# Kernel tuning notes

Hardware: AMD Instinct MI355X
Metric: run time of the kernel (lower is better)

The kernel has to match this reference:

```python
import jax, jax.numpy as jnp
import numpy as np

N = 100000
E = 1600000
FEAT = 128
EMBED = 128
CLASSES = 40


def _sage_conv(x, src, dst, W_l, W_r, b, n_nodes):
    # PyG SAGEConv (mean aggr): out = mean_{j in N(i)} x_j @ W_l + x_i @ W_r + b
    msg = x[src]                                                  # [E, d] gather
    agg = jax.ops.segment_sum(msg, dst, num_segments=n_nodes)     # [N, d]
    cnt = jax.ops.segment_sum(jnp.ones((src.shape[0], 1), x.dtype), dst,
                              num_segments=n_nodes)               # [N, 1]
    agg = agg / jnp.maximum(cnt, 1.0)                             # mean (0 for isolated)
    return agg @ W_l + x @ W_r + b


def setup_inputs() -> dict:
    key = jax.random.key(0)
    ks = jax.random.split(key, 10)
    s = lambda d: 1.0 / np.sqrt(d)
    x = jax.random.normal(ks[0], (N, FEAT), dtype=jnp.float32)
    edge_index = jax.random.randint(ks[1], (2, E), 0, N, dtype=jnp.int64)
    W1_l = jax.random.uniform(ks[2], (FEAT, EMBED), jnp.float32, -s(FEAT), s(FEAT))
    W1_r = jax.random.uniform(ks[3], (FEAT, EMBED), jnp.float32, -s(FEAT), s(FEAT))
    b1 = jnp.zeros((EMBED,), jnp.float32)
    W2_l = jax.random.uniform(ks[4], (EMBED, EMBED), jnp.float32, -s(EMBED), s(EMBED))
    W2_r = jax.random.uniform(ks[5], (EMBED, EMBED), jnp.float32, -s(EMBED), s(EMBED))
    b2 = jnp.zeros((EMBED,), jnp.float32)
    W_out = jax.random.uniform(ks[6], (EMBED, CLASSES), jnp.float32, -s(EMBED), s(EMBED))
    b_out = jax.random.uniform(ks[7], (CLASSES,), jnp.float32, -s(EMBED), s(EMBED))
    return {"x": x, "edge_index": edge_index,
            "W1_l": W1_l, "W1_r": W1_r, "b1": b1,
            "W2_l": W2_l, "W2_r": W2_r, "b2": b2,
            "W_out": W_out, "b_out": b_out}


def reference(x, edge_index, W1_l, W1_r, b1, W2_l, W2_r, b2, W_out, b_out):
    src, dst = edge_index[0], edge_index[1]
    n = x.shape[0]
    h = _sage_conv(x, src, dst, W1_l, W1_r, b1, n)   # [N, EMBED]
    h = _sage_conv(h, src, dst, W2_l, W2_r, b2, n)   # [N, EMBED]
    g = jnp.mean(h, axis=0, keepdims=True)           # global_mean_pool, batch=None -> [1, EMBED]
    return g @ W_out + b_out                          # [1, CLASSES]
```

## Files before the change

### kernel.cpp

```cpp
#include <hip/hip_runtime.h>


#define NN    100000
#define NE    1600000
#define NE4   (NE/4)
#define FEAT  128
#define NCLS  40

#define RSC   25000
#define NRC   4
#define NCC   64
#define PERC  6250

#define RSV   16000
#define NRV   7
#define NCV   32
#define PERV  12500

#define SLICE 200
#define FSG   500
#define P1S   400
#define NV    (3*FEAT + 1)
#define NQ    (P1S / 4)
#define NG    10


__global__ __launch_bounds__(1024) void k_cnt8(const int4* __restrict__ dst4,
                                               unsigned* __restrict__ pc) {
    __shared__ unsigned tab[RSC / 4];
    const int c = blockIdx.x, r = blockIdx.y;
    for (int j = threadIdx.x; j < RSC / 4; j += 1024) tab[j] = 0u;
    __syncthreads();
    const int base = r * RSC;
    const int i0 = c * PERC;
    for (int i = i0 + (int)threadIdx.x; i < i0 + PERC; i += 1024) {
        int4 d = dst4[i];
        unsigned a;
        a = (unsigned)(d.x - base); if (a < RSC) atomicAdd(&tab[a >> 2], 1u << ((a & 3) * 8));
        a = (unsigned)(d.y - base); if (a < RSC) atomicAdd(&tab[a >> 2], 1u << ((a & 3) * 8));
        a = (unsigned)(d.z - base); if (a < RSC) atomicAdd(&tab[a >> 2], 1u << ((a & 3) * 8));
        a = (unsigned)(d.w - base); if (a < RSC) atomicAdd(&tab[a >> 2], 1u << ((a & 3) * 8));
    }
    __syncthreads();
    unsigned* outp = pc + (size_t)(r * NCC + c) * (RSC / 4);
    for (int j = threadIdx.x; j < RSC / 4; j += 1024) outp[j] = tab[j];
}

__global__ __launch_bounds__(256) void k_inv(const unsigned* __restrict__ pc,
                                             float* __restrict__ invc) {
    int i = blockIdx.x * 256 + threadIdx.x;
    if (i >= NN) return;
    int rr = i / RSC, jj = i - rr * RSC;
    const unsigned* p = pc + (size_t)rr * NCC * (RSC / 4) + (jj >> 2);
    const unsigned sh = (unsigned)(jj & 3) * 8u;
    unsigned cn = 0;
    #pragma unroll 16
    for (int c = 0; c < NCC; ++c) cn += (p[(size_t)c * (RSC / 4)] >> sh) & 0xFFu;
    invc[i] = 1.0f / (float)(cn > 0u ? cn : 1u);
}


__global__ __launch_bounds__(1024) void k_scat(const int4* __restrict__ src4,
                                               const int4* __restrict__ dst4,
                                               const float* __restrict__ val,
                                               float* __restrict__ partial) {
    __shared__ float tab[RSV];
    const int c = blockIdx.x, r = blockIdx.y;
    for (int j = threadIdx.x; j < RSV; j += 1024) tab[j] = 0.f;
    __syncthreads();
    const int base = r * RSV;
    const int i0 = c * PERV;
    for (int i = i0 + (int)threadIdx.x; i < i0 + PERV; i += 1024) {
        int4 s = src4[i];
        int4 d = dst4[i];
        unsigned a;
        a = (unsigned)(s.x - base); if (a < RSV) atomicAdd(&tab[a], val[d.x]);
        a = (unsigned)(s.y - base); if (a < RSV) atomicAdd(&tab[a], val[d.y]);
        a = (unsigned)(s.z - base); if (a < RSV) atomicAdd(&tab[a], val[d.z]);
        a = (unsigned)(s.w - base); if (a < RSV) atomicAdd(&tab[a], val[d.w]);
    }
    __syncthreads();
    float* outp = partial + (size_t)(r * NCV + c) * RSV;
    for (int j = threadIdx.x; j < RSV; j += 1024) outp[j] = tab[j];
}

__global__ __launch_bounds__(256) void k_mws(const float* __restrict__ partial,
                                             const float* __restrict__ invc,
                                             float* __restrict__ ws, float* __restrict__ u) {
    int i = blockIdx.x * 256 + threadIdx.x;
    if (i >= NN) return;
    int rr = i / RSV, jj = i - rr * RSV;
    const float* p = partial + (size_t)rr * NCV * RSV + jj;
    float w = 0.f;
    #pragma unroll
    for (int c = 0; c < NCV; ++c) w += p[(size_t)c * RSV];
    ws[i] = w;
    u[i] = w * invc[i];
}


__global__ __launch_bounds__(1024) void k_fsm(const float* __restrict__ x,
                                              const float* __restrict__ ws,
                                              const float* __restrict__ partial,
                                              float* __restrict__ p1) {
    __shared__ float t_sl[SLICE], ws_sl[SLICE];
    __shared__ float shx[32][32][4], shw[32][32][4], sht[32][32][4], wsh[32];
    const int bid = blockIdx.x, tid = threadIdx.x;
    const int i0 = bid * SLICE;
    const int rr = bid / (RSV / SLICE);
    const int jj0 = i0 - rr * RSV;

    if (tid < SLICE) {
        const float* p = partial + (size_t)rr * NCV * RSV + (jj0 + tid);
        float tv = 0.f;
        #pragma unroll
        for (int c = 0; c < NCV; ++c) tv += p[(size_t)c * RSV];
        t_sl[tid] = tv;
        ws_sl[tid] = ws[i0 + tid];
    }
    __syncthreads();

    const int lane = tid & 31;
    const int grp  = tid >> 5;
    float sx0=0,sx1=0,sx2=0,sx3=0;
    float sw0=0,sw1=0,sw2=0,sw3=0;
    float st0=0,st1=0,st2=0,st3=0;
    float wsum = 0.f;
    for (int r = grp; r < SLICE; r += 32) {
        const float4* xr = (const float4*)(x + (size_t)(i0 + r) * FEAT);
        float4 v = xr[lane];
        float wr = ws_sl[r];
        float tr = t_sl[r];
        sx0 += v.x; sx1 += v.y; sx2 += v.z; sx3 += v.w;
        sw0 += wr*v.x; sw1 += wr*v.y; sw2 += wr*v.z; sw3 += wr*v.w;
        st0 += tr*v.x; st1 += tr*v.y; st2 += tr*v.z; st3 += tr*v.w;
        if (lane == 0) wsum += wr;
    }
    shx[grp][lane][0]=sx0; shx[grp][lane][1]=sx1; shx[grp][lane][2]=sx2; shx[grp][lane][3]=sx3;
    shw[grp][lane][0]=sw0; shw[grp][lane][1]=sw1; shw[grp][lane][2]=sw2; shw[grp][lane][3]=sw3;
    sht[grp][lane][0]=st0; sht[grp][lane][1]=st1; sht[grp][lane][2]=st2; sht[grp][lane][3]=st3;
    if (lane == 0) wsh[grp] = wsum;
    __syncthreads();

    if (grp == 0) {
        float ax[4]={0,0,0,0}, aw[4]={0,0,0,0}, at[4]={0,0,0,0};
        for (int g = 0; g < 32; ++g) {
            #pragma unroll
            for (int cc = 0; cc < 4; ++cc) {
                ax[cc] += shx[g][lane][cc];
                aw[cc] += shw[g][lane][cc];
                at[cc] += sht[g][lane][cc];
            }
        }
        float* row = p1 + (size_t)bid * P1S;
        #pragma unroll
        for (int cc = 0; cc < 4; ++cc) {
            row[        4*lane + cc] = ax[cc];
            row[FEAT  + 4*lane + cc] = aw[cc];
            row[2*FEAT+ 4*lane + cc] = at[cc];
        }
        if (lane == 0) {
            float w = 0.f;
            for (int g = 0; g < 32; ++g) w += wsh[g];
            row[3*FEAT] = w;
        }
    }
}


__global__ __launch_bounds__(1024) void k_fin(const float* __restrict__ p1,
                                              const float* __restrict__ W1l, const float* __restrict__ W1r,
                                              const float* __restrict__ b1,
                                              const float* __restrict__ W2l, const float* __restrict__ W2r,
                                              const float* __restrict__ b2,
                                              const float* __restrict__ Wout, const float* __restrict__ bout,
                                              float* __restrict__ out) {
    __shared__ float part[NG][P1S];
    __shared__ float fin[800];
    const int tid = threadIdx.x;

    if (tid < NG * NQ) {
        const int g = tid / NQ;
        const int q = tid - g * NQ;
        const float4* p4 = (const float4*)p1;
        float4 a0 = {0,0,0,0}, a1 = {0,0,0,0};
        const int b0 = g * (FSG / NG);
        #pragma unroll 5
        for (int b = b0; b < b0 + FSG / NG; b += 2) {
            float4 v0 = p4[(size_t)b * NQ + q];
            float4 v1 = p4[(size_t)(b + 1) * NQ + q];
            a0.x += v0.x; a0.y += v0.y; a0.z += v0.z; a0.w += v0.w;
            a1.x += v1.x; a1.y += v1.y; a1.z += v1.z; a1.w += v1.w;
        }
        part[g][4*q    ] = a0.x + a1.x;
        part[g][4*q + 1] = a0.y + a1.y;
        part[g][4*q + 2] = a0.z + a1.z;
        part[g][4*q + 3] = a0.w + a1.w;
    }
    __syncthreads();
    if (tid < NV) {
        float s = 0.f;
        #pragma unroll
        for (int g = 0; g < NG; ++g) s += part[g][tid];
        fin[tid] = s;
    }
    __syncthreads();

    if (tid < FEAT) {
        float m1 = (float)NN * b1[tid];
        float s2 = fin[384] * b1[tid];
        for (int k = 0; k < FEAT; ++k) {
            float wl = W1l[k*FEAT + tid];
            float wr = W1r[k*FEAT + tid];
            m1 += fin[128 + k] * wl + fin[k] * wr;
            s2 += fin[256 + k] * wl + fin[128 + k] * wr;
        }
        fin[400 + tid] = m1;
        fin[528 + tid] = s2;
    }
    __syncthreads();
    if (tid < FEAT) {
        float g = 0.f;
        for (int k = 0; k < FEAT; ++k)
            g += fin[528 + k] * W2l[k*FEAT + tid] + fin[400 + k] * W2r[k*FEAT + tid];
        fin[656 + tid] = g * (1.0f / (float)NN) + b2[tid];
    }
    __syncthreads();
    if (tid < NCLS) {
        float o = bout[tid];
        for (int k = 0; k < FEAT; ++k)
            o += fin[656 + k] * Wout[k*NCLS + tid];
        out[tid] = o;
    }
}


__global__ __launch_bounds__(256) void k_count_dev(const int4* __restrict__ dst4, int* __restrict__ cnt) {
    int i = blockIdx.x * 256 + threadIdx.x;
    if (i >= NE4) return;
    int4 d = dst4[i];
    atomicAdd(&cnt[d.x], 1); atomicAdd(&cnt[d.y], 1);
    atomicAdd(&cnt[d.z], 1); atomicAdd(&cnt[d.w], 1);
}

__global__ __launch_bounds__(256) void k_inv_dev(const int* __restrict__ cnt, float* __restrict__ invc) {
    int i = blockIdx.x * 256 + threadIdx.x;
    if (i >= NN) return;
    int c = cnt[i];
    invc[i] = 1.0f / (float)(c > 0 ? c : 1);
}

__global__ __launch_bounds__(256) void k_ws_dev(const int4* __restrict__ src4, const int4* __restrict__ dst4,
                                                const float* __restrict__ invc, float* __restrict__ ws) {
    int i = blockIdx.x * 256 + threadIdx.x;
    if (i >= NE4) return;
    int4 s = src4[i];
    int4 d = dst4[i];
    atomicAdd(&ws[s.x], invc[d.x]); atomicAdd(&ws[s.y], invc[d.y]);
    atomicAdd(&ws[s.z], invc[d.z]); atomicAdd(&ws[s.w], invc[d.w]);
}

__global__ __launch_bounds__(256) void k_u_dev(const float* __restrict__ ws, const float* __restrict__ invc,
                                               float* __restrict__ u) {
    int i = blockIdx.x * 256 + threadIdx.x;
    if (i >= NN) return;
    u[i] = ws[i] * invc[i];
}

__global__ __launch_bounds__(256) void k_t_dev(const int4* __restrict__ src4, const int4* __restrict__ dst4,
                                               const float* __restrict__ u, float* __restrict__ t) {
    int i = blockIdx.x * 256 + threadIdx.x;
    if (i >= NE4) return;
    int4 s = src4[i];
    int4 d = dst4[i];
    atomicAdd(&t[s.x], u[d.x]); atomicAdd(&t[s.y], u[d.y]);
    atomicAdd(&t[s.z], u[d.z]); atomicAdd(&t[s.w], u[d.w]);
}

__global__ __launch_bounds__(256) void k_fs_atom(const float* __restrict__ x,
                                                 const float* __restrict__ ws,
                                                 const float* __restrict__ t,
                                                 float* __restrict__ sums) {
    int lane = threadIdx.x & 31;
    int grp  = threadIdx.x >> 5;
    int row0 = blockIdx.x * 8 + grp;
    int rstride = gridDim.x * 8;
    float sx0=0,sx1=0,sx2=0,sx3=0, sw0=0,sw1=0,sw2=0,sw3=0, st0=0,st1=0,st2=0,st3=0, wsum=0.f;
    for (int r = row0; r < NN; r += rstride) {
        const float4* xr = (const float4*)(x + (size_t)r * FEAT);
        float4 v = xr[lane];
        float wr = ws[r], tr = t[r];
        sx0+=v.x; sx1+=v.y; sx2+=v.z; sx3+=v.w;
        sw0+=wr*v.x; sw1+=wr*v.y; sw2+=wr*v.z; sw3+=wr*v.w;
        st0+=tr*v.x; st1+=tr*v.y; st2+=tr*v.z; st3+=tr*v.w;
        if (lane==0) wsum += wr;
    }
    __shared__ float shx[8][32][4], shw[8][32][4], sht[8][32][4], shwsum[8];
    shx[grp][lane][0]=sx0; shx[grp][lane][1]=sx1; shx[grp][lane][2]=sx2; shx[grp][lane][3]=sx3;
    shw[grp][lane][0]=sw0; shw[grp][lane][1]=sw1; shw[grp][lane][2]=sw2; shw[grp][lane][3]=sw3;
    sht[grp][lane][0]=st0; sht[grp][lane][1]=st1; sht[grp][lane][2]=st2; sht[grp][lane][3]=st3;
    if (lane==0) shwsum[grp]=wsum;
    __syncthreads();
    if (grp==0) {
        float ax[4], aw[4], at[4];
        #pragma unroll
        for (int c=0;c<4;++c){ax[c]=shx[0][lane][c];aw[c]=shw[0][lane][c];at[c]=sht[0][lane][c];}
        #pragma unroll
        for (int g=1;g<8;++g)
            #pragma unroll
            for (int c=0;c<4;++c){ax[c]+=shx[g][lane][c];aw[c]+=shw[g][lane][c];at[c]+=sht[g][lane][c];}
        #pragma unroll
        for (int c=0;c<4;++c){
            atomicAdd(&sums[        4*lane+c], ax[c]);
            atomicAdd(&sums[FEAT  + 4*lane+c], aw[c]);
            atomicAdd(&sums[2*FEAT+ 4*lane+c], at[c]);
        }
        if (lane==0){
            float w=shwsum[0];
            #pragma unroll
            for (int g=1;g<8;++g) w+=shwsum[g];
            atomicAdd(&sums[3*FEAT], w);
        }
    }
}

__global__ __launch_bounds__(128) void k_final_dev(const float* __restrict__ sums,
                                                   const float* __restrict__ W1l, const float* __restrict__ W1r,
                                                   const float* __restrict__ b1,
                                                   const float* __restrict__ W2l, const float* __restrict__ W2r,
                                                   const float* __restrict__ b2,
                                                   const float* __restrict__ Wout, const float* __restrict__ bout,
                                                   float* __restrict__ out) {
    __shared__ float Sx[FEAT], Sw[FEAT], St[FEAT], M1[FEAT], S2[FEAT], G[FEAT];
    __shared__ float Wsum;
    int f = threadIdx.x;
    Sx[f] = sums[f];
    Sw[f] = sums[FEAT + f];
    St[f] = sums[2*FEAT + f];
    if (f == 0) Wsum = sums[3*FEAT];
    __syncthreads();
    float m1 = (float)NN * b1[f];
    float s2 = Wsum * b1[f];
    for (int k = 0; k < FEAT; ++k) {
        float wl = W1l[k*FEAT + f];
        float wr = W1r[k*FEAT + f];
        m1 += Sw[k]*wl + Sx[k]*wr;
        s2 += St[k]*wl + Sw[k]*wr;
    }
    M1[f] = m1; S2[f] = s2;
    __syncthreads();
    float g = 0.f;
    for (int k = 0; k < FEAT; ++k)
        g += S2[k]*W2l[k*FEAT + f] + M1[k]*W2r[k*FEAT + f];
    g = g * (1.0f/(float)NN) + b2[f];
    G[f] = g;
    __syncthreads();
    if (f < NCLS) {
        float o = bout[f];
        for (int k = 0; k < FEAT; ++k)
            o += G[k]*Wout[k*NCLS + f];
        out[f] = o;
    }
}


extern "C" void kernel_launch(void* const* d_in, const int* in_sizes, int n_in,
                              void* d_out, int out_size, void* d_ws, size_t ws_size,
                              hipStream_t stream) {
    const float* x    = (const float*)d_in[0];
    const int*   ei   = (const int*)d_in[1];
    const float* W1l  = (const float*)d_in[2];
    const float* W1r  = (const float*)d_in[3];
    const float* b1   = (const float*)d_in[4];
    const float* W2l  = (const float*)d_in[5];
    const float* W2r  = (const float*)d_in[6];
    const float* b2   = (const float*)d_in[7];
    const float* Wout = (const float*)d_in[8];
    const float* bout = (const float*)d_in[9];
    float* out = (float*)d_out;

    const int4* src4 = (const int4*)ei;
    const int4* dst4 = (const int4*)(ei + NE);

    const size_t PART = (size_t)NRV * NCV * RSV;
    const size_t P1N  = (size_t)FSG * P1S;
    const size_t need = (PART + (size_t)3*NN + P1N) * 4;

    if (ws_size >= need) {
        float* partial = (float*)d_ws;
        float* invc = partial + PART;
        float* ws   = invc + NN;
        float* u    = ws + NN;
        float* p1   = u + NN;

        const int NB = (NN + 255) / 256;

        k_cnt8<<<dim3(NCC, NRC), 1024, 0, stream>>>(dst4, (unsigned*)partial);
        k_inv<<<NB, 256, 0, stream>>>((const unsigned*)partial, invc);
        k_scat<<<dim3(NCV, NRV), 1024, 0, stream>>>(src4, dst4, invc, partial);
        k_mws<<<NB, 256, 0, stream>>>(partial, invc, ws, u);
        k_scat<<<dim3(NCV, NRV), 1024, 0, stream>>>(src4, dst4, u, partial);
        k_fsm<<<FSG, 1024, 0, stream>>>(x, ws, partial, p1);
        k_fin<<<1, 1024, 0, stream>>>(p1, W1l, W1r, b1, W2l, W2r, b2, Wout, bout, out);
    } else {
        int*   cnt  = (int*)d_ws;
        float* wsv  = (float*)d_ws + NN;
        float* t    = (float*)d_ws + 2*NN;
        float* sums = (float*)d_ws + 3*NN;
        float* invc = (float*)d_ws + 3*NN + 640;
        float* u    = (float*)d_ws + 3*NN + 640 + NN;

        hipMemsetAsync(d_ws, 0, ((size_t)3*NN + 640) * 4, stream);

        const int EB4 = (NE4 + 255) / 256;
        const int NB  = (NN + 255) / 256;
        k_count_dev<<<EB4, 256, 0, stream>>>(dst4, cnt);
        k_inv_dev<<<NB, 256, 0, stream>>>(cnt, invc);
        k_ws_dev<<<EB4, 256, 0, stream>>>(src4, dst4, invc, wsv);
        k_u_dev<<<NB, 256, 0, stream>>>(wsv, invc, u);
        k_t_dev<<<EB4, 256, 0, stream>>>(src4, dst4, u, t);
        k_fs_atom<<<256, 256, 0, stream>>>(x, wsv, t, sums);
        k_final_dev<<<1, 128, 0, stream>>>(sums, W1l, W1r, b1, W2l, W2r, b2, Wout, bout, out);
    }
}
```

Before: 185.7 us.

## Fuse final reduction into k_fsm via last-block pattern and vectorize count/mean kernels

```diff
diff --git a/kernel.cpp b/kernel.cpp
--- a/kernel.cpp
+++ b/kernel.cpp
@@ -26,9 +26,11 @@
 
 
 __global__ __launch_bounds__(1024) void k_cnt8(const int4* __restrict__ dst4,
-                                               unsigned* __restrict__ pc) {
+                                               unsigned* __restrict__ pc,
+                                               unsigned* __restrict__ done) {
     __shared__ unsigned tab[RSC / 4];
     const int c = blockIdx.x, r = blockIdx.y;
+    if (c == 0 && r == 0 && threadIdx.x == 0) *done = 0u;
     for (int j = threadIdx.x; j < RSC / 4; j += 1024) tab[j] = 0u;
     __syncthreads();
     const int base = r * RSC;
@@ -46,17 +48,29 @@
     for (int j = threadIdx.x; j < RSC / 4; j += 1024) outp[j] = tab[j];
 }
 
-__global__ __launch_bounds__(256) void k_inv(const unsigned* __restrict__ pc,
-                                             float* __restrict__ invc) {
-    int i = blockIdx.x * 256 + threadIdx.x;
-    if (i >= NN) return;
-    int rr = i / RSC, jj = i - rr * RSC;
+__global__ __launch_bounds__(256) void k_inv4(const unsigned* __restrict__ pc,
+                                              float* __restrict__ invc) {
+    int i4 = blockIdx.x * 256 + threadIdx.x;
+    if (i4 >= NN / 4) return;
+    const int n0 = i4 * 4;
+    const int rr = n0 / RSC;
+    const int jj = n0 - rr * RSC;
     const unsigned* p = pc + (size_t)rr * NCC * (RSC / 4) + (jj >> 2);
-    const unsigned sh = (unsigned)(jj & 3) * 8u;
-    unsigned cn = 0;
+    unsigned acc02 = 0u, acc13 = 0u;
     #pragma unroll 16
-    for (int c = 0; c < NCC; ++c) cn += (p[(size_t)c * (RSC / 4)] >> sh) & 0xFFu;
-    invc[i] = 1.0f / (float)(cn > 0u ? cn : 1u);
+    for (int c = 0; c < NCC; ++c) {
+        unsigned w = p[(size_t)c * (RSC / 4)];
+        acc02 += w & 0x00FF00FFu;
+        acc13 += (w >> 8) & 0x00FF00FFu;
+    }
+    unsigned c0 = acc02 & 0xFFFFu, c2 = acc02 >> 16;
+    unsigned c1 = acc13 & 0xFFFFu, c3 = acc13 >> 16;
+    float4 v;
+    v.x = 1.0f / (float)(c0 > 0u ? c0 : 1u);
+    v.y = 1.0f / (float)(c1 > 0u ? c1 : 1u);
+    v.z = 1.0f / (float)(c2 > 0u ? c2 : 1u);
+    v.w = 1.0f / (float)(c3 > 0u ? c3 : 1u);
+    ((float4*)invc)[i4] = v;
 }
 
 
@@ -84,40 +98,67 @@
     for (int j = threadIdx.x; j < RSV; j += 1024) outp[j] = tab[j];
 }
 
-__global__ __launch_bounds__(256) void k_mws(const float* __restrict__ partial,
-                                             const float* __restrict__ invc,
-                                             float* __restrict__ ws, float* __restrict__ u) {
-    int i = blockIdx.x * 256 + threadIdx.x;
-    if (i >= NN) return;
-    int rr = i / RSV, jj = i - rr * RSV;
-    const float* p = partial + (size_t)rr * NCV * RSV + jj;
-    float w = 0.f;
-    #pragma unroll
-    for (int c = 0; c < NCV; ++c) w += p[(size_t)c * RSV];
-    ws[i] = w;
-    u[i] = w * invc[i];
+__global__ __launch_bounds__(256) void k_mws4(const float* __restrict__ partial,
+                                              const float* __restrict__ invc,
+                                              float* __restrict__ ws, float* __restrict__ u) {
+    int i4 = blockIdx.x * 256 + threadIdx.x;
+    if (i4 >= NN / 4) return;
+    const int n0 = i4 * 4;
+    const int rr = n0 / RSV;
+    const int jj = n0 - rr * RSV;
+    const float4* p = (const float4*)(partial + (size_t)rr * NCV * RSV + jj);
+    float4 w = {0.f, 0.f, 0.f, 0.f};
+    #pragma unroll 8
+    for (int c = 0; c < NCV; ++c) {
+        float4 v = p[(size_t)c * (RSV / 4)];
+        w.x += v.x; w.y += v.y; w.z += v.z; w.w += v.w;
+    }
+    ((float4*)ws)[i4] = w;
+    float4 ic = ((const float4*)invc)[i4];
+    float4 uu = {w.x * ic.x, w.y * ic.y, w.z * ic.z, w.w * ic.w};
+    ((float4*)u)[i4] = uu;
 }
 
 
 __global__ __launch_bounds__(1024) void k_fsm(const float* __restrict__ x,
                                               const float* __restrict__ ws,
                                               const float* __restrict__ partial,
-                                              float* __restrict__ p1) {
-    __shared__ float t_sl[SLICE], ws_sl[SLICE];
-    __shared__ float shx[32][32][4], shw[32][32][4], sht[32][32][4], wsh[32];
+                                              float* __restrict__ p1,
+                                              unsigned* __restrict__ done,
+                                              const float* __restrict__ W1l, const float* __restrict__ W1r,
+                                              const float* __restrict__ b1,
+                                              const float* __restrict__ W2l, const float* __restrict__ W2r,
+                                              const float* __restrict__ b2,
+                                              const float* __restrict__ Wout, const float* __restrict__ bout,
+                                              float* __restrict__ out) {
+    __shared__ float smem[13520];
+    __shared__ unsigned s_last;
+    float* t_sl  = smem;
+    float* ws_sl = smem + 200;
+    float* wsh   = smem + 400;
+    float* tpart = smem + 432;
+    float* shx   = smem + 1232;
+    float* shw   = smem + 5328;
+    float* sht   = smem + 9424;
+
     const int bid = blockIdx.x, tid = threadIdx.x;
     const int i0 = bid * SLICE;
     const int rr = bid / (RSV / SLICE);
     const int jj0 = i0 - rr * RSV;
 
-    if (tid < SLICE) {
-        const float* p = partial + (size_t)rr * NCV * RSV + (jj0 + tid);
+    if (tid < 4 * SLICE) {
+        const int g = tid / SLICE;
+        const int n = tid - g * SLICE;
+        const float* p = partial + (size_t)rr * NCV * RSV + (size_t)(g * 8) * RSV + (jj0 + n);
         float tv = 0.f;
         #pragma unroll
-        for (int c = 0; c < NCV; ++c) tv += p[(size_t)c * RSV];
-        t_sl[tid] = tv;
-        ws_sl[tid] = ws[i0 + tid];
-    }
+        for (int c = 0; c < 8; ++c) tv += p[(size_t)c * RSV];
+        tpart[g * SLICE + n] = tv;
+    }
+    if (tid < SLICE) ws_sl[tid] = ws[i0 + tid];
+    __syncthreads();
+    if (tid < SLICE)
+        t_sl[tid] = tpart[tid] + tpart[SLICE + tid] + tpart[2 * SLICE + tid] + tpart[3 * SLICE + tid];
     __syncthreads();
 
     const int lane = tid & 31;
@@ -136,9 +177,12 @@
         st0 += tr*v.x; st1 += tr*v.y; st2 += tr*v.z; st3 += tr*v.w;
         if (lane == 0) wsum += wr;
     }
-    shx[grp][lane][0]=sx0; shx[grp][lane][1]=sx1; shx[grp][lane][2]=sx2; shx[grp][lane][3]=sx3;
-    shw[grp][lane][0]=sw0; shw[grp][lane][1]=sw1; shw[grp][lane][2]=sw2; shw[grp][lane][3]=sw3;
-    sht[grp][lane][0]=st0; sht[grp][lane][1]=st1; sht[grp][lane][2]=st2; sht[grp][lane][3]=st3;
+    float* px = shx + grp * 128 + lane * 4;
+    float* pw = shw + grp * 128 + lane * 4;
+    float* pt = sht + grp * 128 + lane * 4;
+    px[0]=sx0; px[1]=sx1; px[2]=sx2; px[3]=sx3;
+    pw[0]=sw0; pw[1]=sw1; pw[2]=sw2; pw[3]=sw3;
+    pt[0]=st0; pt[1]=st1; pt[2]=st2; pt[3]=st3;
     if (lane == 0) wsh[grp] = wsum;
     __syncthreads();
 
@@ -147,9 +191,9 @@
         for (int g = 0; g < 32; ++g) {
             #pragma unroll
             for (int cc = 0; cc < 4; ++cc) {
-                ax[cc] += shx[g][lane][cc];
-                aw[cc] += shw[g][lane][cc];
-                at[cc] += sht[g][lane][cc];
+                ax[cc] += shx[g*128 + lane*4 + cc];
+                aw[cc] += shw[g*128 + lane*4 + cc];
+                at[cc] += sht[g*128 + lane*4 + cc];
             }
         }
         float* row = p1 + (size_t)bid * P1S;
@@ -165,19 +209,22 @@
             row[3*FEAT] = w;
         }
     }
-}
-
-
-__global__ __launch_bounds__(1024) void k_fin(const float* __restrict__ p1,
-                                              const float* __restrict__ W1l, const float* __restrict__ W1r,
-                                              const float* __restrict__ b1,
-                                              const float* __restrict__ W2l, const float* __restrict__ W2r,
-                                              const float* __restrict__ b2,
-                                              const float* __restrict__ Wout, const float* __restrict__ bout,
-                                              float* __restrict__ out) {
-    __shared__ float part[NG][P1S];
-    __shared__ float fin[800];
-    const int tid = threadIdx.x;
+    __syncthreads();
+
+    if (tid == 0) {
+        __threadfence();
+        unsigned old = atomicAdd(done, 1u);
+        s_last = (old == (unsigned)(FSG - 1)) ? 1u : 0u;
+    }
+    __syncthreads();
+    if (!s_last) return;
+    __threadfence();
+
+    float* part = smem;
+    float* fin  = smem + 4000;
+    float* pm   = smem + 4800;
+    float* ps   = smem + 5824;
+    float* po   = smem + 6848;
 
     if (tid < NG * NQ) {
         const int g = tid / NQ;
@@ -192,44 +239,73 @@
             a0.x += v0.x; a0.y += v0.y; a0.z += v0.z; a0.w += v0.w;
             a1.x += v1.x; a1.y += v1.y; a1.z += v1.z; a1.w += v1.w;
         }
-        part[g][4*q    ] = a0.x + a1.x;
-        part[g][4*q + 1] = a0.y + a1.y;
-        part[g][4*q + 2] = a0.z + a1.z;
-        part[g][4*q + 3] = a0.w + a1.w;
+        part[g*P1S + 4*q    ] = a0.x + a1.x;
+        part[g*P1S + 4*q + 1] = a0.y + a1.y;
+        part[g*P1S + 4*q + 2] = a0.z + a1.z;
+        part[g*P1S + 4*q + 3] = a0.w + a1.w;
     }
     __syncthreads();
     if (tid < NV) {
         float s = 0.f;
         #pragma unroll
-        for (int g = 0; g < NG; ++g) s += part[g][tid];
+        for (int g = 0; g < NG; ++g) s += part[g*P1S + tid];
         fin[tid] = s;
     }
     __syncthreads();
 
+    const int f  = tid & 127;
+    const int g8 = tid >> 7;
+    const int k0 = g8 * 16;
+
+    {
+        float m1 = 0.f, s2 = 0.f;
+        #pragma unroll
+        for (int k = k0; k < k0 + 16; ++k) {
+            float wl = W1l[k*FEAT + f];
+            float wr = W1r[k*FEAT + f];
+            m1 += fin[128 + k] * wl + fin[k] * wr;
+            s2 += fin[256 + k] * wl + fin[128 + k] * wr;
+        }
+        pm[g8*128 + f] = m1;
+        ps[g8*128 + f] = s2;
+    }
+    __syncthreads();
     if (tid < FEAT) {
         float m1 = (float)NN * b1[tid];
         float s2 = fin[384] * b1[tid];
-        for (int k = 0; k < FEAT; ++k) {
-            float wl = W1l[k*FEAT + tid];
-            float wr = W1r[k*FEAT + tid];
-            m1 += fin[128 + k] * wl + fin[k] * wr;
-            s2 += fin[256 + k] * wl + fin[128 + k] * wr;
-        }
+        #pragma unroll
+        for (int g = 0; g < 8; ++g) { m1 += pm[g*128 + tid]; s2 += ps[g*128 + tid]; }
         fin[400 + tid] = m1;
         fin[528 + tid] = s2;
     }
     __syncthreads();
+    {
+        float gg = 0.f;
+        #pragma unroll
+        for (int k = k0; k < k0 + 16; ++k)
+            gg += fin[528 + k] * W2l[k*FEAT + f] + fin[400 + k] * W2r[k*FEAT + f];
+        pm[g8*128 + f] = gg;
+    }
+    __syncthreads();
     if (tid < FEAT) {
-        float g = 0.f;
-        for (int k = 0; k < FEAT; ++k)
-            g += fin[528 + k] * W2l[k*FEAT + tid] + fin[400 + k] * W2r[k*FEAT + tid];
-        fin[656 + tid] = g * (1.0f / (float)NN) + b2[tid];
+        float gg = 0.f;
+        #pragma unroll
+        for (int g = 0; g < 8; ++g) gg += pm[g*128 + tid];
+        fin[656 + tid] = gg * (1.0f / (float)NN) + b2[tid];
+    }
+    __syncthreads();
+    if (f < NCLS) {
+        float o = 0.f;
+        #pragma unroll
+        for (int k = k0; k < k0 + 16; ++k)
+            o += fin[656 + k] * Wout[k*NCLS + f];
+        po[g8*40 + f] = o;
     }
     __syncthreads();
     if (tid < NCLS) {
         float o = bout[tid];
-        for (int k = 0; k < FEAT; ++k)
-            o += fin[656 + k] * Wout[k*NCLS + tid];
+        #pragma unroll
+        for (int g = 0; g < 8; ++g) o += po[g*40 + tid];
         out[tid] = o;
     }
 }
@@ -384,7 +460,7 @@
 
     const size_t PART = (size_t)NRV * NCV * RSV;
     const size_t P1N  = (size_t)FSG * P1S;
-    const size_t need = (PART + (size_t)3*NN + P1N) * 4;
+    const size_t need = (PART + (size_t)3*NN + P1N + 16) * 4;
 
     if (ws_size >= need) {
         float* partial = (float*)d_ws;
@@ -392,16 +468,17 @@
         float* ws   = invc + NN;
         float* u    = ws + NN;
         float* p1   = u + NN;
-
-        const int NB = (NN + 255) / 256;
-
-        k_cnt8<<<dim3(NCC, NRC), 1024, 0, stream>>>(dst4, (unsigned*)partial);
-        k_inv<<<NB, 256, 0, stream>>>((const unsigned*)partial, invc);
+        unsigned* done = (unsigned*)(p1 + P1N);
+
+        const int NB4 = (NN/4 + 255) / 256;
+
+        k_cnt8<<<dim3(NCC, NRC), 1024, 0, stream>>>(dst4, (unsigned*)partial, done);
+        k_inv4<<<NB4, 256, 0, stream>>>((const unsigned*)partial, invc);
         k_scat<<<dim3(NCV, NRV), 1024, 0, stream>>>(src4, dst4, invc, partial);
-        k_mws<<<NB, 256, 0, stream>>>(partial, invc, ws, u);
+        k_mws4<<<NB4, 256, 0, stream>>>(partial, invc, ws, u);
         k_scat<<<dim3(NCV, NRV), 1024, 0, stream>>>(src4, dst4, u, partial);
-        k_fsm<<<FSG, 1024, 0, stream>>>(x, ws, partial, p1);
-        k_fin<<<1, 1024, 0, stream>>>(p1, W1l, W1r, b1, W2l, W2r, b2, Wout, bout, out);
+        k_fsm<<<FSG, 1024, 0, stream>>>(x, ws, partial, p1, done,
+                                        W1l, W1r, b1, W2l, W2r, b2, Wout, bout, out);
     } else {
         int*   cnt  = (int*)d_ws;
         float* wsv  = (float*)d_ws + NN;
```

New measurement: 196.3 us. +5.7%, slower.
